# Kernel tuning notes

Hardware: AMD Instinct MI355X
Metric: run time of the kernel (lower is better)

## Reference

```python
import jax, jax.numpy as jnp
import numpy as np

D = 512       # d_model
M = 64        # working memory_dim
SE = 32       # episodic slots
SS = 64       # semantic slots
H = 4         # episodic heads
B, L = 2, 1024
BOT = max(D // 4, 32)  # controller bottleneck = 128


def _layernorm(x, g, b, eps=1e-5):
    mu = jnp.mean(x, axis=-1, keepdims=True)
    var = jnp.var(x, axis=-1, keepdims=True)
    return (x - mu) * jax.lax.rsqrt(var + eps) * g + b


def setup_inputs() -> dict:
    key = jax.random.key(0)
    ks = jax.random.split(key, 24)
    r = lambda i, shape, s=0.02: jax.random.normal(ks[i], shape, dtype=jnp.float32) * s
    return {
        "x": jax.random.normal(ks[0], (B, L, D), dtype=jnp.float32),
        # WorkingMemory (weights stored as (in, out))
        "Wq": r(1, (D, M)), "Wk": r(2, (D, M)), "Wv": r(3, (D, D)),
        "Wf": r(4, (D, M)), "bf": jnp.zeros((M,), jnp.float32),
        "Wo": r(5, (D, D)),
        "ln_g": jnp.ones((D,), jnp.float32), "ln_b": jnp.zeros((D,), jnp.float32),
        # EpisodicMemory
        "eslots": r(6, (1, SE, D)),
        "Eq": r(7, (D, D)), "Ek": r(8, (D, D)), "Ev": r(9, (D, D)), "Eo": r(10, (D, D)),
        # SemanticMemory
        "know": r(11, (1, SS, D)),
        "Sin": r(12, (D, D)),
        "Sg_w": r(13, (D, D)), "Sg_b": jnp.zeros((D,), jnp.float32),
        "So": r(14, (D, D)),
        # MemoryController
        "C1w": r(15, (D, BOT)), "C1b": jnp.zeros((BOT,), jnp.float32),
        "C2w": r(16, (BOT, 3)), "C2b": jnp.zeros((3,), jnp.float32),
    }


def _forward(x, Wq, Wk, Wv, Wf, bf, Wo, ln_g, ln_b,
             eslots, Eq, Ek, Ev, Eo,
             know, Sin, Sg_w, Sg_b, So,
             C1w, C1b, C2w, C2b):
    b, l, d = x.shape
    # ---- WorkingMemory (parallel gated linear attention) ----
    scale = M ** -0.5
    q = (jax.nn.elu(x @ Wq) + 1.0) * scale          # (B,L,M)
    k = jax.nn.elu(x @ Wk) + 1.0                    # (B,L,M)
    v = x @ Wv                                      # (B,L,D)
    forget = jax.nn.sigmoid(x @ Wf + bf)            # (B,L,M)
    log_f_cum = jnp.clip(jnp.cumsum(jnp.log(jnp.clip(forget, 1e-6, None)), axis=1), -20.0, 20.0)
    exp_neg = jnp.exp(-log_f_cum)
    exp_pos = jnp.exp(log_f_cum)
    kv = k[..., :, None] * v[..., None, :]          # (B,L,M,D) outer product
    cum_kv = jnp.cumsum(exp_neg[..., None] * kv, axis=1)
    Mstate = exp_pos[..., None] * cum_kv            # (B,L,M,D)
    z = exp_pos * jnp.cumsum(exp_neg * k, axis=1)   # (B,L,M)
    num = jnp.einsum('blm,blmd->bld', q, Mstate)
    den = jnp.einsum('blm,blm->bl', q, z)[..., None] + 1e-6
    w_out = _layernorm(num / den, ln_g, ln_b) @ Wo  # (B,L,D)

    # ---- EpisodicMemory (cross-attn to learned slots) ----
    hd = D // H
    mem = jnp.broadcast_to(eslots, (b, SE, D))
    qh = (x @ Eq).reshape(b, l, H, hd)
    kh = (mem @ Ek).reshape(b, SE, H, hd)
    vh = (mem @ Ev).reshape(b, SE, H, hd)
    scores = jnp.einsum('blhe,bshe->bhls', qh, kh) / jnp.sqrt(jnp.float32(hd))
    attn = jax.nn.softmax(scores, axis=-1)
    e_out = jnp.einsum('bhls,bshe->blhe', attn, vh).reshape(b, l, D) @ Eo

    # ---- SemanticMemory (single-head attn to knowledge, gated residual) ----
    kb = jnp.broadcast_to(know, (b, SS, D))
    qs = x @ Sin                                    # (B,L,D)
    s_scores = jnp.einsum('bld,bsd->bls', qs, kb) / jnp.sqrt(jnp.float32(D))
    s_attn = jax.nn.softmax(s_scores, axis=-1)
    retrieved = jnp.einsum('bls,bsd->bld', s_attn, kb)
    gate = jax.nn.sigmoid(x @ Sg_w + Sg_b)
    s_out = (gate * retrieved + (1.0 - gate) * x) @ So

    # ---- Controller fusion ----
    wts = jax.nn.softmax(jax.nn.silu(x @ C1w + C1b) @ C2w + C2b, axis=-1)  # (B,L,3)
    fused = (wts[..., 0:1] * w_out + wts[..., 1:2] * e_out + wts[..., 2:3] * s_out)
    return fused


def reference(x, Wq, Wk, Wv, Wf, bf, Wo, ln_g, ln_b,
              eslots, Eq, Ek, Ev, Eo,
              know, Sin, Sg_w, Sg_b, So,
              C1w, C1b, C2w, C2b):
    return _forward(x, Wq, Wk, Wv, Wf, bf, Wo, ln_g, ln_b,
                    eslots, Eq, Ek, Ev, Eo,
                    know, Sin, Sg_w, Sg_b, So,
                    C1w, C1b, C2w, C2b)
```

## Files before the change

### kernel.cpp

```cpp
#include <hip/hip_runtime.h>
#include <cstdint>

typedef unsigned int uint;
typedef unsigned short ushort;
typedef __attribute__((ext_vector_type(8))) short bf16x8;
typedef __attribute__((ext_vector_type(4))) float f32x4;

__device__ __forceinline__ ushort f2b(float f) {
  union { float f; uint u; } v; v.f = f;
  uint u = v.u;
  uint r = (u + 0x7FFFu + ((u >> 16) & 1u)) >> 16;
  return (ushort)r;
}
__device__ __forceinline__ float b2f(ushort h) {
  union { uint u; float f; } v; v.u = ((uint)h) << 16; return v.f;
}

__global__ __launch_bounds__(256) void k_prep(
    const float* __restrict__ x, const float* __restrict__ Wv, const float* __restrict__ Sg,
    const float* __restrict__ C1w, const float* __restrict__ Wq, const float* __restrict__ Wk,
    const float* __restrict__ Wo, const float* __restrict__ So, const float* __restrict__ know,
    const float* __restrict__ eslots, const float* __restrict__ Ek, const float* __restrict__ Ev,
    const float* __restrict__ Sin, const float* __restrict__ Wf, const float* __restrict__ bfb,
    ushort* __restrict__ X16, ushort* __restrict__ Wcat, ushort* __restrict__ Wfin,
    ushort* __restrict__ know16, float* __restrict__ kh, float* __restrict__ vh,
    float* __restrict__ logfb)
{
  __shared__ __align__(16) float Af[16 * 32];
  __shared__ __align__(16) float Bf[32 * 64];
  __shared__ __align__(16) float T[64][65];
  int bid = blockIdx.x;
  int tid = threadIdx.x;
  int lane = tid & 63, wv = tid >> 6;

  if (bid < 128) {
    int r0 = bid * 16;
    int row = tid >> 4, col4 = (tid & 15) * 4;
    float a0 = 0.f, a1 = 0.f, a2 = 0.f, a3 = 0.f;
    for (int kt = 0; kt < 16; ++kt) {
      if (tid < 128) {
        int p = tid; int rr = p >> 3, c4 = (p & 7) * 4;
        *(float4*)&Af[rr * 32 + c4] = *(const float4*)&x[(size_t)(r0 + rr) * 512 + kt * 32 + c4];
      }
      #pragma unroll
      for (int i = 0; i < 2; ++i) {
        int p = i * 256 + tid; int rr = p >> 4, c4 = (p & 15) * 4;
        *(float4*)&Bf[rr * 64 + c4] = *(const float4*)&Wf[(size_t)(kt * 32 + rr) * 64 + c4];
      }
      __syncthreads();
      #pragma unroll 8
      for (int ks = 0; ks < 32; ++ks) {
        float a = Af[row * 32 + ks];
        float4 b = *(float4*)&Bf[ks * 64 + col4];
        a0 += a * b.x; a1 += a * b.y; a2 += a * b.z; a3 += a * b.w;
      }
      __syncthreads();
    }
    float accs[4] = {a0, a1, a2, a3};
    #pragma unroll
    for (int j = 0; j < 4; ++j) {
      float logit = accs[j] + bfb[col4 + j];
      float s = 1.f / (1.f + expf(-logit));
      logfb[(size_t)(r0 + row) * 64 + col4 + j] = logf(fmaxf(s, 1e-6f));
    }
    return;
  }
  if (bid < 256) {
    int t = (bid - 128) * 256 + tid;
    if (t < 16384) {
      int s = t >> 9, j = t & 511;
      float acc = 0.f;
      #pragma unroll 8
      for (int d = 0; d < 512; ++d) acc += eslots[s * 512 + d] * Ek[d * 512 + j];
      kh[s * 512 + j] = acc;
    } else {
      int o = t - 16384; int s = o >> 9, j = o & 511;
      float acc = 0.f;
      #pragma unroll 8
      for (int d = 0; d < 512; ++d) acc += eslots[s * 512 + d] * Ev[d * 512 + j];
      vh[s * 512 + j] = acc;
    }
    return;
  }
  if (bid < 384) {
    int k = (bid - 256) * 4 + wv;
    const float* sp = Sin + (size_t)k * 512 + lane * 8;
    float4 s1 = *(const float4*)&sp[0];
    float4 s2 = *(const float4*)&sp[4];
    for (int s = 0; s < 64; ++s) {
      const float* kp = know + (size_t)s * 512 + lane * 8;
      float4 k1 = *(const float4*)&kp[0];
      float4 k2 = *(const float4*)&kp[4];
      float part = s1.x * k1.x + s1.y * k1.y + s1.z * k1.z + s1.w * k1.w
                 + s2.x * k2.x + s2.y * k2.y + s2.z * k2.z + s2.w * k2.w;
      #pragma unroll
      for (int o = 32; o; o >>= 1) part += __shfl_xor(part, o);
      if (lane == 0) Wcat[(640 + s) * 512 + k] = f2b(part * 0.04419417382415922f);
    }
    return;
  }
  if (bid < 672) {
    int tt = bid - 384;
    const float* src; ushort* dst; int sld, dld, Nt, drow, dcol;
    if (tt < 64)       {           src = Wv;  dst = Wcat; sld = 512; dld = 512;  Nt = 8; drow = 0;    dcol = 0;   }
    else if (tt < 128) { tt -= 64; src = Sg;  dst = Wcat; sld = 512; dld = 512;  Nt = 8; drow = 704;  dcol = 0;   }
    else if (tt < 144) { tt -= 128; src = C1w; dst = Wcat; sld = 128; dld = 512; Nt = 2; drow = 1216; dcol = 0;   }
    else if (tt < 152) { tt -= 144; src = Wq;  dst = Wcat; sld = 64;  dld = 512; Nt = 1; drow = 1344; dcol = 0;   }
    else if (tt < 160) { tt -= 152; src = Wk;  dst = Wcat; sld = 64;  dld = 512; Nt = 1; drow = 1408; dcol = 0;   }
    else if (tt < 224) { tt -= 160; src = Wo;  dst = Wfin; sld = 512; dld = 1152; Nt = 8; drow = 0;   dcol = 0;   }
    else               { tt -= 224; src = So;  dst = Wfin; sld = 512; dld = 1152; Nt = 8; drow = 0;   dcol = 512; }
    int tk = tt / Nt, tn = tt % Nt;
    int k0 = tk * 64, n0 = tn * 64;
    int r = tid >> 4, c = (tid & 15) * 4;
    #pragma unroll
    for (int p = 0; p < 4; ++p) {
      int kk = p * 16 + r;
      float4 v = *(const float4*)&src[(size_t)(k0 + kk) * sld + n0 + c];
      T[c + 0][kk] = v.x; T[c + 1][kk] = v.y; T[c + 2][kk] = v.z; T[c + 3][kk] = v.w;
    }
    __syncthreads();
    int n = tid >> 2, kc = (tid & 3) * 16;
    uint u[8];
    #pragma unroll
    for (int j = 0; j < 8; ++j) {
      ushort lo = f2b(T[n][kc + 2 * j]);
      ushort hi = f2b(T[n][kc + 2 * j + 1]);
      u[j] = (uint)lo | ((uint)hi << 16);
    }
    size_t off = (size_t)(drow + n0 + n) * dld + dcol + k0 + kc;
    uint4 o1; o1.x = u[0]; o1.y = u[1]; o1.z = u[2]; o1.w = u[3];
    uint4 o2; o2.x = u[4]; o2.y = u[5]; o2.z = u[6]; o2.w = u[7];
    *(uint4*)&dst[off] = o1;
    *(uint4*)&dst[off + 8] = o2;
    return;
  }
  if (bid < 800) {
    int base = (bid - 672) * 256 + tid;
    #pragma unroll
    for (int it = 0; it < 8; ++it) {
      int t = base + it * 32768;
      float4 xv = *(const float4*)&x[(size_t)t * 4];
      uint2 o;
      o.x = (uint)f2b(xv.x) | ((uint)f2b(xv.y) << 16);
      o.y = (uint)f2b(xv.z) | ((uint)f2b(xv.w) << 16);
      *(uint2*)&X16[(size_t)t * 4] = o;
    }
    return;
  }
  {
    int t = (bid - 800) * 256 + tid;
    #pragma unroll
    for (int j = 0; j < 2; ++j) {
      float4 v = *(const float4*)&know[(size_t)t * 8 + j * 4];
      uint2 o;
      o.x = (uint)f2b(v.x) | ((uint)f2b(v.y) << 16);
      o.y = (uint)f2b(v.z) | ((uint)f2b(v.w) << 16);
      *(uint2*)&know16[(size_t)t * 8 + j * 4] = o;
    }
  }
}

__global__ __launch_bounds__(256) void k_pre2(
    const float* __restrict__ Eq, const float* __restrict__ kh, const float* __restrict__ vh,
    const float* __restrict__ Eo, ushort* __restrict__ Wcat, ushort* __restrict__ Wfin)
{
  int bid = blockIdx.x;
  int tid = threadIdx.x;
  int lane = tid & 63, wv = tid >> 6;
  if (bid < 256) {
    int gw = bid * 4 + wv;
    #pragma unroll
    for (int pp = 0; pp < 2; ++pp) {
      int pair = gw * 2 + pp;
      int k = pair >> 2, h = pair & 3;
      const float* ep = Eq + (size_t)k * 512 + h * 128 + lane * 2;
      float e0 = ep[0], e1 = ep[1];
      for (int s = 0; s < 32; ++s) {
        const float* kp = kh + (size_t)s * 512 + h * 128 + lane * 2;
        float part = e0 * kp[0] + e1 * kp[1];
        #pragma unroll
        for (int o = 32; o; o >>= 1) part += __shfl_xor(part, o);
        if (lane == 0) Wcat[(512 + h * 32 + s) * 512 + k] = f2b(part * 0.08838834764831845f);
      }
    }
  } else {
    int o = (bid - 256) * 256 + tid;
    int hs = o >> 9, j = o & 511;
    int h = hs >> 5, s = hs & 31;
    const float* vhp = vh + (size_t)s * 512 + h * 128;
    float acc = 0.f;
    #pragma unroll 8
    for (int e = 0; e < 128; ++e) acc += vhp[e] * Eo[(size_t)(h * 128 + e) * 512 + j];
    Wfin[(size_t)j * 1152 + 1024 + hs] = f2b(acc);
  }
}

__global__ __launch_bounds__(256) void k_gemm1(
    const ushort* __restrict__ A, const ushort* __restrict__ Bw, float* __restrict__ C,
    const float* __restrict__ sgb, const float* __restrict__ c1b)
{
  __shared__ __align__(16) ushort As[64 * 32];
  __shared__ __align__(16) ushort Bs[128 * 32];
  int tid = threadIdx.x;
  int lane = tid & 63, wv = tid >> 6;
  int wm = (wv & 1) * 32, wn = (wv >> 1) * 64;
  int lr = lane & 15, lk = lane >> 4;
  int m0 = blockIdx.y * 64, n0 = blockIdx.x * 128;
  f32x4 zero4 = {0.f, 0.f, 0.f, 0.f};
  f32x4 acc[2][4];
  #pragma unroll
  for (int a = 0; a < 2; ++a)
    #pragma unroll
    for (int b = 0; b < 4; ++b) acc[a][b] = zero4;
  for (int kt = 0; kt < 16; ++kt) {
    int k0 = kt * 32;
    {
      int p = tid, row = p >> 2, cc = p & 3;
      int cs = cc ^ ((row >> 1) & 3);
      *(uint4*)&As[p * 8] = *(const uint4*)&A[(size_t)(m0 + row) * 512 + k0 + cs * 8];
    }
    #pragma unroll
    for (int i = 0; i < 2; ++i) {
      int p = i * 256 + tid, row = p >> 2, cc = p & 3;
      int cs = cc ^ ((row >> 1) & 3);
      *(uint4*)&Bs[p * 8] = *(const uint4*)&Bw[(size_t)(n0 + row) * 512 + k0 + cs * 8];
    }
    __syncthreads();
    bf16x8 af[2], bfv[4];
    #pragma unroll
    for (int mi = 0; mi < 2; ++mi) {
      int row = wm + mi * 16 + lr;
      int cc = lk ^ ((row >> 1) & 3);
      af[mi] = *(bf16x8*)&As[row * 32 + cc * 8];
    }
    #pragma unroll
    for (int ni = 0; ni < 4; ++ni) {
      int row = wn + ni * 16 + lr;
      int cc = lk ^ ((row >> 1) & 3);
      bfv[ni] = *(bf16x8*)&Bs[row * 32 + cc * 8];
    }
    #pragma unroll
    for (int mi = 0; mi < 2; ++mi)
      #pragma unroll
      for (int ni = 0; ni < 4; ++ni)
        acc[mi][ni] = __builtin_amdgcn_mfma_f32_16x16x32_bf16(af[mi], bfv[ni], acc[mi][ni], 0, 0, 0);
    __syncthreads();
  }
  #pragma unroll
  for (int mi = 0; mi < 2; ++mi) {
    #pragma unroll
    for (int ni = 0; ni < 4; ++ni) {
      int col = n0 + wn + ni * 16 + lr;
      #pragma unroll
      for (int r = 0; r < 4; ++r) {
        int rowb = m0 + wm + mi * 16 + lk * 4 + r;
        float v = acc[mi][ni][r];
        if (col >= 704) {
          if (col < 1216) { v = 1.f / (1.f + __expf(-(v + sgb[col - 704]))); }
          else if (col < 1344) { float tt = v + c1b[col - 1216]; v = tt / (1.f + __expf(-tt)); }
          else if (col < 1408) { float e = (v > 0.f) ? v : (__expf(v) - 1.f); v = (e + 1.f) * 0.125f; }
          else if (col < 1472) { float e = (v > 0.f) ? v : (__expf(v) - 1.f); v = e + 1.f; }
        }
        C[(size_t)rowb * 1536 + col] = v;
      }
    }
  }
}

__global__ __launch_bounds__(256) void k_gemm2(
    const ushort* __restrict__ A, const ushort* __restrict__ Bw, float* __restrict__ C)
{
  __shared__ __align__(16) ushort As[64 * 32];
  __shared__ __align__(16) ushort Bs[64 * 32];
  int tid = threadIdx.x;
  int lane = tid & 63, wv = tid >> 6;
  int wm = (wv & 1) * 32, wn = (wv >> 1) * 32;
  int lr = lane & 15, lk = lane >> 4;
  int m0 = blockIdx.y * 64, n0 = blockIdx.x * 64;
  f32x4 zero4 = {0.f, 0.f, 0.f, 0.f};
  f32x4 acc[2][2];
  #pragma unroll
  for (int a = 0; a < 2; ++a)
    #pragma unroll
    for (int b = 0; b < 2; ++b) acc[a][b] = zero4;
  for (int kt = 0; kt < 36; ++kt) {
    int k0 = kt * 32;
    {
      int p = tid, row = p >> 2, cc = p & 3;
      int cs = cc ^ ((row >> 1) & 3);
      *(uint4*)&As[p * 8] = *(const uint4*)&A[(size_t)(m0 + row) * 1152 + k0 + cs * 8];
      *(uint4*)&Bs[p * 8] = *(const uint4*)&Bw[(size_t)(n0 + row) * 1152 + k0 + cs * 8];
    }
    __syncthreads();
    bf16x8 af[2], bfv[2];
    #pragma unroll
    for (int mi = 0; mi < 2; ++mi) {
      int row = wm + mi * 16 + lr;
      int cc = lk ^ ((row >> 1) & 3);
      af[mi] = *(bf16x8*)&As[row * 32 + cc * 8];
    }
    #pragma unroll
    for (int ni = 0; ni < 2; ++ni) {
      int row = wn + ni * 16 + lr;
      int cc = lk ^ ((row >> 1) & 3);
      bfv[ni] = *(bf16x8*)&Bs[row * 32 + cc * 8];
    }
    #pragma unroll
    for (int mi = 0; mi < 2; ++mi)
      #pragma unroll
      for (int ni = 0; ni < 2; ++ni)
        acc[mi][ni] = __builtin_amdgcn_mfma_f32_16x16x32_bf16(af[mi], bfv[ni], acc[mi][ni], 0, 0, 0);
    __syncthreads();
  }
  #pragma unroll
  for (int mi = 0; mi < 2; ++mi) {
    #pragma unroll
    for (int ni = 0; ni < 2; ++ni) {
      int col = n0 + wn + ni * 16 + lr;
      #pragma unroll
      for (int r = 0; r < 4; ++r) {
        int rowb = m0 + wm + mi * 16 + lk * 4 + r;
        C[(size_t)rowb * 512 + col] = acc[mi][ni][r];
      }
    }
  }
}

__global__ __launch_bounds__(256) void k_gatescan(
    const float* __restrict__ logfb, const float* __restrict__ P,
    float* __restrict__ cn, float* __restrict__ qe, float* __restrict__ qz)
{
  __shared__ float wsumA[4];
  __shared__ float wsumB[4];
  int bidx = blockIdx.x;
  int b = bidx >> 6, m = bidx & 63;
  int tid = threadIdx.x;
  int lane = tid & 63, wv = tid >> 6;
  size_t rbase = (size_t)b * 1024 + tid * 4;

  float v0 = logfb[(rbase + 0) * 64 + m];
  float v1 = logfb[(rbase + 1) * 64 + m];
  float v2 = logfb[(rbase + 2) * 64 + m];
  float v3 = logfb[(rbase + 3) * 64 + m];
  v1 += v0; v2 += v1; v3 += v2;
  float tsum = v3;
  float sc = tsum;
  #pragma unroll
  for (int o = 1; o < 64; o <<= 1) {
    float t = __shfl_up(sc, o, 64);
    if (lane >= o) sc += t;
  }
  if (lane == 63) wsumA[wv] = sc;
  __syncthreads();
  float excl = sc - tsum;
  #pragma unroll
  for (int w2 = 0; w2 < 3; ++w2) if (w2 < wv) excl += wsumA[w2];

  float vv[4] = {v0, v1, v2, v3};
  float cv[4], qv[4];
  #pragma unroll
  for (int i = 0; i < 4; ++i) {
    size_t r = rbase + i;
    float lf = fminf(fmaxf(excl + vv[i], -20.f), 20.f);
    float en = expf(-lf), ep = expf(lf);
    float kk = P[r * 1536 + 1408 + m];
    float qq = P[r * 1536 + 1344 + m];
    cv[i] = en * kk;
    qv[i] = qq * ep;
    cn[r * 64 + m] = cv[i];
    qe[r * 64 + m] = qv[i];
  }

  float c1 = cv[0], c2 = c1 + cv[1], c3 = c2 + cv[2], c4 = c3 + cv[3];
  float t2 = c4;
  float sc2 = t2;
  #pragma unroll
  for (int o = 1; o < 64; o <<= 1) {
    float t = __shfl_up(sc2, o, 64);
    if (lane >= o) sc2 += t;
  }
  if (lane == 63) wsumB[wv] = sc2;
  __syncthreads();
  float excl2 = sc2 - t2;
  #pragma unroll
  for (int w2 = 0; w2 < 3; ++w2) if (w2 < wv) excl2 += wsumB[w2];

  float pr[4] = {c1, c2, c3, c4};
  #pragma unroll
  for (int i = 0; i < 4; ++i) {
    size_t r = rbase + i;
    qz[r * 64 + m] = qv[i] * (excl2 + pr[i]);
  }
}

__global__ __launch_bounds__(256) void k_scanA(
    const float* __restrict__ cn, const float* __restrict__ P, float* __restrict__ Send)
{
  __shared__ __align__(16) float cnS[16 * 64];
  __shared__ __align__(16) float vS[16 * 64];
  int tid = threadIdx.x;
  int bid = blockIdx.x;
  int dt = bid & 7, c = (bid >> 3) & 15, b = bid >> 7;
  int rb0 = b * 1024 + c * 64;
  int mg = tid >> 4, dl = tid & 15;
  float4 acc[4];
  #pragma unroll
  for (int i = 0; i < 4; ++i) acc[i] = make_float4(0.f, 0.f, 0.f, 0.f);
  for (int ig = 0; ig < 4; ++ig) {
    int rb = rb0 + ig * 16;
    int row = tid >> 4, c4f = (tid & 15) * 4;
    *(float4*)&cnS[row * 64 + c4f] = *(const float4*)&cn[(size_t)(rb + row) * 64 + c4f];
    *(float4*)&vS[row * 64 + c4f] = *(const float4*)&P[(size_t)(rb + row) * 1536 + dt * 64 + c4f];
    __syncthreads();
    #pragma unroll 4
    for (int i = 0; i < 16; ++i) {
      float4 vv = *(float4*)&vS[i * 64 + dl * 4];
      float4 cm = *(float4*)&cnS[i * 64 + mg * 4];
      acc[0].x += cm.x * vv.x; acc[0].y += cm.x * vv.y; acc[0].z += cm.x * vv.z; acc[0].w += cm.x * vv.w;
      acc[1].x += cm.y * vv.x; acc[1].y += cm.y * vv.y; acc[1].z += cm.y * vv.z; acc[1].w += cm.y * vv.w;
      acc[2].x += cm.z * vv.x; acc[2].y += cm.z * vv.y; acc[2].z += cm.z * vv.z; acc[2].w += cm.z * vv.w;
      acc[3].x += cm.w * vv.x; acc[3].y += cm.w * vv.y; acc[3].z += cm.w * vv.z; acc[3].w += cm.w * vv.w;
    }
    __syncthreads();
  }
  #pragma unroll
  for (int mi = 0; mi < 4; ++mi) {
    int m = mg * 4 + mi;
    *(float4*)&Send[(size_t)((b * 16 + c) * 64 + m) * 512 + dt * 64 + dl * 4] = acc[mi];
  }
}

__global__ __launch_bounds__(256) void k_scanB(const float* __restrict__ Send, float* __restrict__ carry)
{
  int t = blockIdx.x * 256 + threadIdx.x;
  int d = t & 511, m = (t >> 9) & 63, b = t >> 15;
  float run = 0.f;
  for (int c = 0; c < 16; ++c) {
    size_t idx = (size_t)((b * 16 + c) * 64 + m) * 512 + d;
    carry[idx] = run;
    run += Send[idx];
  }
}

__global__ __launch_bounds__(256) void k_scanC(
    const float* __restrict__ cn, const float* __restrict__ qe, const float* __restrict__ P,
    const float* __restrict__ carry, float* __restrict__ num)
{
  __shared__ __align__(16) float cnS[16 * 64];
  __shared__ __align__(16) float qeS[16 * 64];
  __shared__ __align__(16) float vS[16 * 64];
  int tid = threadIdx.x;
  int bid = blockIdx.x;
  int dt = bid & 7, c = (bid >> 3) & 15, b = bid >> 7;
  int rb0 = b * 1024 + c * 64;
  int mg = tid & 3, dl = tid >> 2;
  int d = dt * 64 + dl;
  float S[16];
  #pragma unroll
  for (int mi = 0; mi < 16; ++mi)
    S[mi] = carry[(size_t)((b * 16 + c) * 64 + mg * 16 + mi) * 512 + d];
  for (int ig = 0; ig < 4; ++ig) {
    int rb = rb0 + ig * 16;
    int row = tid >> 4, c4f = (tid & 15) * 4;
    *(float4*)&cnS[row * 64 + c4f] = *(const float4*)&cn[(size_t)(rb + row) * 64 + c4f];
    *(float4*)&qeS[row * 64 + c4f] = *(const float4*)&qe[(size_t)(rb + row) * 64 + c4f];
    *(float4*)&vS[row * 64 + c4f] = *(const float4*)&P[(size_t)(rb + row) * 1536 + dt * 64 + c4f];
    __syncthreads();
    for (int i = 0; i < 16; ++i) {
      float vv = vS[i * 64 + dl];
      float p = 0.f;
      #pragma unroll
      for (int j = 0; j < 4; ++j) {
        float4 c4 = *(float4*)&cnS[i * 64 + mg * 16 + j * 4];
        float4 q4 = *(float4*)&qeS[i * 64 + mg * 16 + j * 4];
        S[j * 4 + 0] += c4.x * vv; p += q4.x * S[j * 4 + 0];
        S[j * 4 + 1] += c4.y * vv; p += q4.y * S[j * 4 + 1];
        S[j * 4 + 2] += c4.z * vv; p += q4.z * S[j * 4 + 2];
        S[j * 4 + 3] += c4.w * vv; p += q4.w * S[j * 4 + 3];
      }
      p += __shfl_xor(p, 1);
      p += __shfl_xor(p, 2);
      if (mg == 0) num[(size_t)(rb + i) * 512 + d] = p;
    }
    __syncthreads();
  }
}

__global__ __launch_bounds__(256) void k_post(
    const float* __restrict__ P, const float* __restrict__ x,
    const float* __restrict__ num, const float* __restrict__ qz,
    const ushort* __restrict__ know16, const float* __restrict__ lng,
    const float* __restrict__ lnb, const float* __restrict__ C2w,
    const float* __restrict__ C2b, ushort* __restrict__ Afin)
{
  __shared__ __align__(16) ushort kbuf[32 * 512];
  __shared__ float attnL[4][64];
  __shared__ float w2L[4];
  int tid = threadIdx.x;
  int w = tid >> 6, lane = tid & 63;
  int r0 = blockIdx.x * 4;
  int r = r0 + w;
  size_t pr = (size_t)r * 1536;

  float h0 = P[pr + 1216 + lane], h1 = P[pr + 1280 + lane];
  float a0 = h0 * C2w[lane * 3 + 0] + h1 * C2w[(64 + lane) * 3 + 0];
  float a1 = h0 * C2w[lane * 3 + 1] + h1 * C2w[(64 + lane) * 3 + 1];
  float a2 = h0 * C2w[lane * 3 + 2] + h1 * C2w[(64 + lane) * 3 + 2];
  #pragma unroll
  for (int o = 32; o; o >>= 1) {
    a0 += __shfl_xor(a0, o); a1 += __shfl_xor(a1, o); a2 += __shfl_xor(a2, o);
  }
  a0 += C2b[0]; a1 += C2b[1]; a2 += C2b[2];
  float mxc = fmaxf(a0, fmaxf(a1, a2));
  float e0 = expf(a0 - mxc), e1 = expf(a1 - mxc), e2c = expf(a2 - mxc);
  float inv = 1.f / (e0 + e1 + e2c);
  float w0 = e0 * inv, w1 = e1 * inv, w2 = e2c * inv;
  if (lane == 0) w2L[w] = w2;

  {
    float den = qz[(size_t)r * 64 + lane];
    #pragma unroll
    for (int o = 32; o; o >>= 1) den += __shfl_xor(den, o);
    den += 1e-6f;
    float y[8];
    float4 n0 = *(const float4*)&num[(size_t)r * 512 + lane * 8];
    float4 n1 = *(const float4*)&num[(size_t)r * 512 + lane * 8 + 4];
    y[0] = n0.x / den; y[1] = n0.y / den; y[2] = n0.z / den; y[3] = n0.w / den;
    y[4] = n1.x / den; y[5] = n1.y / den; y[6] = n1.z / den; y[7] = n1.w / den;
    float s1 = 0.f, s2 = 0.f;
    #pragma unroll
    for (int i = 0; i < 8; ++i) { s1 += y[i]; s2 += y[i] * y[i]; }
    #pragma unroll
    for (int o = 32; o; o >>= 1) { s1 += __shfl_xor(s1, o); s2 += __shfl_xor(s2, o); }
    float mu = s1 * (1.f / 512.f);
    float var = s2 * (1.f / 512.f) - mu * mu;
    float rs = rsqrtf(var + 1e-5f);
    uint4 outv;
    uint pk[4];
    #pragma unroll
    for (int p2 = 0; p2 < 4; ++p2) {
      float o0 = (y[2 * p2] - mu) * rs * lng[lane * 8 + 2 * p2] + lnb[lane * 8 + 2 * p2];
      float o1 = (y[2 * p2 + 1] - mu) * rs * lng[lane * 8 + 2 * p2 + 1] + lnb[lane * 8 + 2 * p2 + 1];
      pk[p2] = (uint)f2b(o0 * w0) | ((uint)f2b(o1 * w0) << 16);
    }
    outv.x = pk[0]; outv.y = pk[1]; outv.z = pk[2]; outv.w = pk[3];
    *(uint4*)&Afin[(size_t)r * 1152 + lane * 8] = outv;
  }

  {
    int h = lane >> 4, ei = (lane & 15) * 2;
    float v0 = P[pr + 512 + h * 32 + ei], v1 = P[pr + 512 + h * 32 + ei + 1];
    float mxe = fmaxf(v0, v1);
    #pragma unroll
    for (int o = 1; o < 16; o <<= 1) mxe = fmaxf(mxe, __shfl_xor(mxe, o));
    float ee0 = __expf(v0 - mxe), ee1 = __expf(v1 - mxe);
    float ss = ee0 + ee1;
    #pragma unroll
    for (int o = 1; o < 16; o <<= 1) ss += __shfl_xor(ss, o);
    float sc1 = w1 / ss;
    uint pkv = (uint)f2b(ee0 * sc1) | ((uint)f2b(ee1 * sc1) << 16);
    *(uint*)&Afin[(size_t)r * 1152 + 1024 + h * 32 + ei] = pkv;
  }

  {
    float lv = P[pr + 640 + lane];
    float mx = lv;
    #pragma unroll
    for (int o = 32; o; o >>= 1) mx = fmaxf(mx, __shfl_xor(mx, o));
    float e = __expf(lv - mx);
    float sum = e;
    #pragma unroll
    for (int o = 32; o; o >>= 1) sum += __shfl_xor(sum, o);
    attnL[w][lane] = e / sum;
  }

  int dd = tid * 2;
  float acc[4][2];
  #pragma unroll
  for (int i = 0; i < 4; ++i) { acc[i][0] = 0.f; acc[i][1] = 0.f; }
  for (int hs = 0; hs < 2; ++hs) {
    #pragma unroll
    for (int i = 0; i < 8; ++i) {
      int idx = i * 256 + tid;
      *(uint4*)&kbuf[idx * 8] = *(const uint4*)&know16[(size_t)hs * 16384 + idx * 8];
    }
    __syncthreads();
    for (int s = 0; s < 32; ++s) {
      uint uu = *(uint*)&kbuf[s * 512 + dd];
      float k0 = b2f((ushort)(uu & 0xffff));
      float k1 = b2f((ushort)(uu >> 16));
      #pragma unroll
      for (int row = 0; row < 4; ++row) {
        float a = attnL[row][hs * 32 + s];
        acc[row][0] += a * k0;
        acc[row][1] += a * k1;
      }
    }
    __syncthreads();
  }
  #pragma unroll
  for (int row = 0; row < 4; ++row) {
    int rr = r0 + row;
    float g0 = P[(size_t)rr * 1536 + 704 + dd];
    float g1 = P[(size_t)rr * 1536 + 704 + dd + 1];
    float x0 = x[(size_t)rr * 512 + dd], x1 = x[(size_t)rr * 512 + dd + 1];
    float w2v = w2L[row];
    float m0 = g0 * acc[row][0] + (1.f - g0) * x0;
    float m1 = g1 * acc[row][1] + (1.f - g1) * x1;
    uint pkv = (uint)f2b(w2v * m0) | ((uint)f2b(w2v * m1) << 16);
    *(uint*)&Afin[(size_t)rr * 1152 + 512 + dd] = pkv;
  }
}

extern "C" void kernel_launch(void* const* d_in, const int* in_sizes, int n_in,
                              void* d_out, int out_size, void* d_ws, size_t ws_size,
                              hipStream_t stream)
{
  const float* x     = (const float*)d_in[0];
  const float* Wq    = (const float*)d_in[1];
  const float* Wk    = (const float*)d_in[2];
  const float* Wv    = (const float*)d_in[3];
  const float* Wf    = (const float*)d_in[4];
  const float* bfb   = (const float*)d_in[5];
  const float* Wo    = (const float*)d_in[6];
  const float* ln_g  = (const float*)d_in[7];
  const float* ln_b  = (const float*)d_in[8];
  const float* eslots= (const float*)d_in[9];
  const float* Eq    = (const float*)d_in[10];
  const float* Ek    = (const float*)d_in[11];
  const float* Ev    = (const float*)d_in[12];
  const float* Eo    = (const float*)d_in[13];
  const float* know  = (const float*)d_in[14];
  const float* Sin   = (const float*)d_in[15];
  const float* Sg_w  = (const float*)d_in[16];
  const float* Sg_b  = (const float*)d_in[17];
  const float* So    = (const float*)d_in[18];
  const float* C1w   = (const float*)d_in[19];
  const float* C1b   = (const float*)d_in[20];
  const float* C2w   = (const float*)d_in[21];
  const float* C2b   = (const float*)d_in[22];

  char* ws = (char*)d_ws;
  ushort* X16    = (ushort*)(ws + 0);
  ushort* Wcat   = (ushort*)(ws + 2097152);
  ushort* Wfin   = (ushort*)(ws + 3670016);
  ushort* know16 = (ushort*)(ws + 4849664);
  float*  kh     = (float*)(ws + 4915200);
  float*  vh     = (float*)(ws + 4980736);
  float*  P      = (float*)(ws + 5046272);
  float*  logfb  = (float*)(ws + 17629184);
  float*  cn     = (float*)(ws + 18153472);
  float*  qe     = (float*)(ws + 18677760);
  float*  qz     = (float*)(ws + 19202048);
  float*  Send   = (float*)(ws + 19726336);
  float*  carry  = (float*)(ws + 23920640);
  float*  num    = (float*)(ws + 28114944);
  ushort* Afin   = (ushort*)(ws + 32342016);

  k_prep<<<dim3(816), dim3(256), 0, stream>>>(x, Wv, Sg_w, C1w, Wq, Wk, Wo, So, know,
                                              eslots, Ek, Ev, Sin, Wf, bfb,
                                              X16, Wcat, Wfin, know16, kh, vh, logfb);
  k_pre2<<<dim3(512), dim3(256), 0, stream>>>(Eq, kh, vh, Eo, Wcat, Wfin);
  k_gemm1<<<dim3(12, 32), dim3(256), 0, stream>>>(X16, Wcat, P, Sg_b, C1b);
  k_gatescan<<<dim3(128), dim3(256), 0, stream>>>(logfb, P, cn, qe, qz);
  k_scanA<<<dim3(256), dim3(256), 0, stream>>>(cn, P, Send);
  k_scanB<<<dim3(256), dim3(256), 0, stream>>>(Send, carry);
  k_scanC<<<dim3(256), dim3(256), 0, stream>>>(cn, qe, P, carry, num);
  k_post<<<dim3(512), dim3(256), 0, stream>>>(P, x, num, qz, know16, ln_g, ln_b, C2w, C2b, Afin);
  k_gemm2<<<dim3(8, 32), dim3(256), 0, stream>>>(Afin, Wfin, (float*)d_out);
}
```

Measured before the change: 145.3 us.

## Fuse gate scan into chunked scan kernels and drop carry pass

```diff
diff --git a/kernel.cpp b/kernel.cpp
--- a/kernel.cpp
+++ b/kernel.cpp
@@ -24,7 +24,7 @@
     const float* __restrict__ Sin, const float* __restrict__ Wf, const float* __restrict__ bfb,
     ushort* __restrict__ X16, ushort* __restrict__ Wcat, ushort* __restrict__ Wfin,
     ushort* __restrict__ know16, float* __restrict__ kh, float* __restrict__ vh,
-    float* __restrict__ logfb)
+    float* __restrict__ logfb, float* __restrict__ s16)
 {
   __shared__ __align__(16) float Af[16 * 32];
   __shared__ __align__(16) float Bf[32 * 64];
@@ -57,11 +57,22 @@
       __syncthreads();
     }
     float accs[4] = {a0, a1, a2, a3};
+    float lv[4];
     #pragma unroll
     for (int j = 0; j < 4; ++j) {
       float logit = accs[j] + bfb[col4 + j];
       float s = 1.f / (1.f + expf(-logit));
-      logfb[(size_t)(r0 + row) * 64 + col4 + j] = logf(fmaxf(s, 1e-6f));
+      lv[j] = logf(fmaxf(s, 1e-6f));
+      logfb[(size_t)(r0 + row) * 64 + col4 + j] = lv[j];
+    }
+    #pragma unroll
+    for (int j = 0; j < 4; ++j) Bf[row * 64 + col4 + j] = lv[j];
+    __syncthreads();
+    if (tid < 64) {
+      float s = 0.f;
+      #pragma unroll
+      for (int rr = 0; rr < 16; ++rr) s += Bf[rr * 64 + tid];
+      s16[(size_t)bid * 64 + tid] = s;
     }
     return;
   }
@@ -326,82 +337,38 @@
   }
 }
 
-__global__ __launch_bounds__(256) void k_gatescan(
-    const float* __restrict__ logfb, const float* __restrict__ P,
-    float* __restrict__ cn, float* __restrict__ qe, float* __restrict__ qz)
-{
-  __shared__ float wsumA[4];
-  __shared__ float wsumB[4];
-  int bidx = blockIdx.x;
-  int b = bidx >> 6, m = bidx & 63;
-  int tid = threadIdx.x;
-  int lane = tid & 63, wv = tid >> 6;
-  size_t rbase = (size_t)b * 1024 + tid * 4;
-
-  float v0 = logfb[(rbase + 0) * 64 + m];
-  float v1 = logfb[(rbase + 1) * 64 + m];
-  float v2 = logfb[(rbase + 2) * 64 + m];
-  float v3 = logfb[(rbase + 3) * 64 + m];
-  v1 += v0; v2 += v1; v3 += v2;
-  float tsum = v3;
-  float sc = tsum;
-  #pragma unroll
-  for (int o = 1; o < 64; o <<= 1) {
-    float t = __shfl_up(sc, o, 64);
-    if (lane >= o) sc += t;
-  }
-  if (lane == 63) wsumA[wv] = sc;
-  __syncthreads();
-  float excl = sc - tsum;
-  #pragma unroll
-  for (int w2 = 0; w2 < 3; ++w2) if (w2 < wv) excl += wsumA[w2];
-
-  float vv[4] = {v0, v1, v2, v3};
-  float cv[4], qv[4];
-  #pragma unroll
-  for (int i = 0; i < 4; ++i) {
-    size_t r = rbase + i;
-    float lf = fminf(fmaxf(excl + vv[i], -20.f), 20.f);
-    float en = expf(-lf), ep = expf(lf);
-    float kk = P[r * 1536 + 1408 + m];
-    float qq = P[r * 1536 + 1344 + m];
-    cv[i] = en * kk;
-    qv[i] = qq * ep;
-    cn[r * 64 + m] = cv[i];
-    qe[r * 64 + m] = qv[i];
-  }
-
-  float c1 = cv[0], c2 = c1 + cv[1], c3 = c2 + cv[2], c4 = c3 + cv[3];
-  float t2 = c4;
-  float sc2 = t2;
-  #pragma unroll
-  for (int o = 1; o < 64; o <<= 1) {
-    float t = __shfl_up(sc2, o, 64);
-    if (lane >= o) sc2 += t;
-  }
-  if (lane == 63) wsumB[wv] = sc2;
-  __syncthreads();
-  float excl2 = sc2 - t2;
-  #pragma unroll
-  for (int w2 = 0; w2 < 3; ++w2) if (w2 < wv) excl2 += wsumB[w2];
-
-  float pr[4] = {c1, c2, c3, c4};
-  #pragma unroll
-  for (int i = 0; i < 4; ++i) {
-    size_t r = rbase + i;
-    qz[r * 64 + m] = qv[i] * (excl2 + pr[i]);
-  }
-}
-
 __global__ __launch_bounds__(256) void k_scanA(
-    const float* __restrict__ cn, const float* __restrict__ P, float* __restrict__ Send)
-{
-  __shared__ __align__(16) float cnS[16 * 64];
+    const float* __restrict__ logfb, const float* __restrict__ s16,
+    const float* __restrict__ P, float* __restrict__ Send, float* __restrict__ zSend)
+{
+  __shared__ __align__(16) float cnS[64 * 64];
+  __shared__ __align__(16) float kS[64 * 64];
   __shared__ __align__(16) float vS[16 * 64];
   int tid = threadIdx.x;
   int bid = blockIdx.x;
   int dt = bid & 7, c = (bid >> 3) & 15, b = bid >> 7;
   int rb0 = b * 1024 + c * 64;
+  for (int idx = tid; idx < 1024; idx += 256) {
+    int i = idx >> 4, m4 = (idx & 15) * 4;
+    *(float4*)&cnS[i * 64 + m4] = *(const float4*)&logfb[(size_t)(rb0 + i) * 64 + m4];
+    *(float4*)&kS[i * 64 + m4] = *(const float4*)&P[(size_t)(rb0 + i) * 1536 + 1408 + m4];
+  }
+  __syncthreads();
+  if (tid < 64) {
+    int m = tid;
+    float run = 0.f;
+    for (int j = 0; j < c * 4; ++j) run += s16[(size_t)(b * 64 + j) * 64 + m];
+    float zs = 0.f;
+    for (int i = 0; i < 64; ++i) {
+      run += cnS[i * 64 + m];
+      float lf = fminf(fmaxf(run, -20.f), 20.f);
+      float cv = __expf(-lf) * kS[i * 64 + m];
+      cnS[i * 64 + m] = cv;
+      zs += cv;
+    }
+    if (dt == 0) zSend[(size_t)(b * 16 + c) * 64 + m] = zs;
+  }
+  __syncthreads();
   int mg = tid >> 4, dl = tid & 15;
   float4 acc[4];
   #pragma unroll
@@ -409,13 +376,12 @@
   for (int ig = 0; ig < 4; ++ig) {
     int rb = rb0 + ig * 16;
     int row = tid >> 4, c4f = (tid & 15) * 4;
-    *(float4*)&cnS[row * 64 + c4f] = *(const float4*)&cn[(size_t)(rb + row) * 64 + c4f];
     *(float4*)&vS[row * 64 + c4f] = *(const float4*)&P[(size_t)(rb + row) * 1536 + dt * 64 + c4f];
     __syncthreads();
     #pragma unroll 4
     for (int i = 0; i < 16; ++i) {
       float4 vv = *(float4*)&vS[i * 64 + dl * 4];
-      float4 cm = *(float4*)&cnS[i * 64 + mg * 4];
+      float4 cm = *(float4*)&cnS[(ig * 16 + i) * 64 + mg * 4];
       acc[0].x += cm.x * vv.x; acc[0].y += cm.x * vv.y; acc[0].z += cm.x * vv.z; acc[0].w += cm.x * vv.w;
       acc[1].x += cm.y * vv.x; acc[1].y += cm.y * vv.y; acc[1].z += cm.y * vv.z; acc[1].w += cm.y * vv.w;
       acc[2].x += cm.z * vv.x; acc[2].y += cm.z * vv.y; acc[2].z += cm.z * vv.z; acc[2].w += cm.z * vv.w;
@@ -430,57 +396,86 @@
   }
 }
 
-__global__ __launch_bounds__(256) void k_scanB(const float* __restrict__ Send, float* __restrict__ carry)
-{
-  int t = blockIdx.x * 256 + threadIdx.x;
-  int d = t & 511, m = (t >> 9) & 63, b = t >> 15;
-  float run = 0.f;
-  for (int c = 0; c < 16; ++c) {
-    size_t idx = (size_t)((b * 16 + c) * 64 + m) * 512 + d;
-    carry[idx] = run;
-    run += Send[idx];
-  }
-}
-
 __global__ __launch_bounds__(256) void k_scanC(
-    const float* __restrict__ cn, const float* __restrict__ qe, const float* __restrict__ P,
-    const float* __restrict__ carry, float* __restrict__ num)
-{
-  __shared__ __align__(16) float cnS[16 * 64];
-  __shared__ __align__(16) float qeS[16 * 64];
+    const float* __restrict__ logfb, const float* __restrict__ s16,
+    const float* __restrict__ P, const float* __restrict__ Send,
+    const float* __restrict__ zSend, float* __restrict__ num, float* __restrict__ den)
+{
+  __shared__ __align__(16) float cnS[64 * 64];
+  __shared__ __align__(16) float qeS[64 * 64];
+  __shared__ __align__(16) float kS[64 * 64];
   __shared__ __align__(16) float vS[16 * 64];
   int tid = threadIdx.x;
   int bid = blockIdx.x;
   int dt = bid & 7, c = (bid >> 3) & 15, b = bid >> 7;
   int rb0 = b * 1024 + c * 64;
+  for (int idx = tid; idx < 1024; idx += 256) {
+    int i = idx >> 4, m4 = (idx & 15) * 4;
+    *(float4*)&cnS[i * 64 + m4] = *(const float4*)&logfb[(size_t)(rb0 + i) * 64 + m4];
+    *(float4*)&kS[i * 64 + m4] = *(const float4*)&P[(size_t)(rb0 + i) * 1536 + 1408 + m4];
+    *(float4*)&qeS[i * 64 + m4] = *(const float4*)&P[(size_t)(rb0 + i) * 1536 + 1344 + m4];
+  }
+  __syncthreads();
+  if (tid < 64) {
+    int m = tid;
+    float run = 0.f;
+    for (int j = 0; j < c * 4; ++j) run += s16[(size_t)(b * 64 + j) * 64 + m];
+    for (int i = 0; i < 64; ++i) {
+      run += cnS[i * 64 + m];
+      float lf = fminf(fmaxf(run, -20.f), 20.f);
+      float ep = __expf(lf), en = __expf(-lf);
+      cnS[i * 64 + m] = en * kS[i * 64 + m];
+      qeS[i * 64 + m] = qeS[i * 64 + m] * ep;
+    }
+  }
+  __syncthreads();
   int mg = tid & 3, dl = tid >> 2;
   int d = dt * 64 + dl;
   float S[16];
-  #pragma unroll
-  for (int mi = 0; mi < 16; ++mi)
-    S[mi] = carry[(size_t)((b * 16 + c) * 64 + mg * 16 + mi) * 512 + d];
+  float z16[16];
+  #pragma unroll
+  for (int mi = 0; mi < 16; ++mi) { S[mi] = 0.f; z16[mi] = 0.f; }
+  for (int j = 0; j < c; ++j) {
+    size_t base = (size_t)((b * 16 + j) * 64 + mg * 16) * 512 + d;
+    #pragma unroll
+    for (int mi = 0; mi < 16; ++mi) S[mi] += Send[base + (size_t)mi * 512];
+    size_t zb = (size_t)(b * 16 + j) * 64 + mg * 16;
+    #pragma unroll
+    for (int mi = 0; mi < 16; ++mi) z16[mi] += zSend[zb + mi];
+  }
   for (int ig = 0; ig < 4; ++ig) {
     int rb = rb0 + ig * 16;
     int row = tid >> 4, c4f = (tid & 15) * 4;
-    *(float4*)&cnS[row * 64 + c4f] = *(const float4*)&cn[(size_t)(rb + row) * 64 + c4f];
-    *(float4*)&qeS[row * 64 + c4f] = *(const float4*)&qe[(size_t)(rb + row) * 64 + c4f];
     *(float4*)&vS[row * 64 + c4f] = *(const float4*)&P[(size_t)(rb + row) * 1536 + dt * 64 + c4f];
     __syncthreads();
     for (int i = 0; i < 16; ++i) {
+      int ii = ig * 16 + i;
       float vv = vS[i * 64 + dl];
       float p = 0.f;
+      float dp = 0.f;
       #pragma unroll
       for (int j = 0; j < 4; ++j) {
-        float4 c4 = *(float4*)&cnS[i * 64 + mg * 16 + j * 4];
-        float4 q4 = *(float4*)&qeS[i * 64 + mg * 16 + j * 4];
+        float4 c4 = *(float4*)&cnS[ii * 64 + mg * 16 + j * 4];
+        float4 q4 = *(float4*)&qeS[ii * 64 + mg * 16 + j * 4];
         S[j * 4 + 0] += c4.x * vv; p += q4.x * S[j * 4 + 0];
         S[j * 4 + 1] += c4.y * vv; p += q4.y * S[j * 4 + 1];
         S[j * 4 + 2] += c4.z * vv; p += q4.z * S[j * 4 + 2];
         S[j * 4 + 3] += c4.w * vv; p += q4.w * S[j * 4 + 3];
+        if (dt == 0) {
+          z16[j * 4 + 0] += c4.x; dp += q4.x * z16[j * 4 + 0];
+          z16[j * 4 + 1] += c4.y; dp += q4.y * z16[j * 4 + 1];
+          z16[j * 4 + 2] += c4.z; dp += q4.z * z16[j * 4 + 2];
+          z16[j * 4 + 3] += c4.w; dp += q4.w * z16[j * 4 + 3];
+        }
       }
       p += __shfl_xor(p, 1);
       p += __shfl_xor(p, 2);
-      if (mg == 0) num[(size_t)(rb + i) * 512 + d] = p;
+      if (mg == 0) num[(size_t)(rb0 + ii) * 512 + d] = p;
+      if (dt == 0) {
+        dp += __shfl_xor(dp, 1);
+        dp += __shfl_xor(dp, 2);
+        if (mg == 0 && dl == 0) den[rb0 + ii] = dp;
+      }
     }
     __syncthreads();
   }
@@ -488,7 +483,7 @@
 
 __global__ __launch_bounds__(256) void k_post(
     const float* __restrict__ P, const float* __restrict__ x,
-    const float* __restrict__ num, const float* __restrict__ qz,
+    const float* __restrict__ num, const float* __restrict__ denB,
     const ushort* __restrict__ know16, const float* __restrict__ lng,
     const float* __restrict__ lnb, const float* __restrict__ C2w,
     const float* __restrict__ C2b, ushort* __restrict__ Afin)
@@ -518,15 +513,12 @@
   if (lane == 0) w2L[w] = w2;
 
   {
-    float den = qz[(size_t)r * 64 + lane];
-    #pragma unroll
-    for (int o = 32; o; o >>= 1) den += __shfl_xor(den, o);
-    den += 1e-6f;
+    float dv = denB[r] + 1e-6f;
     float y[8];
     float4 n0 = *(const float4*)&num[(size_t)r * 512 + lane * 8];
     float4 n1 = *(const float4*)&num[(size_t)r * 512 + lane * 8 + 4];
-    y[0] = n0.x / den; y[1] = n0.y / den; y[2] = n0.z / den; y[3] = n0.w / den;
-    y[4] = n1.x / den; y[5] = n1.y / den; y[6] = n1.z / den; y[7] = n1.w / den;
+    y[0] = n0.x / dv; y[1] = n0.y / dv; y[2] = n0.z / dv; y[3] = n0.w / dv;
+    y[4] = n1.x / dv; y[5] = n1.y / dv; y[6] = n1.z / dv; y[7] = n1.w / dv;
     float s1 = 0.f, s2 = 0.f;
     #pragma unroll
     for (int i = 0; i < 8; ++i) { s1 += y[i]; s2 += y[i] * y[i]; }
@@ -649,23 +641,20 @@
   float*  vh     = (float*)(ws + 4980736);
   float*  P      = (float*)(ws + 5046272);
   float*  logfb  = (float*)(ws + 17629184);
-  float*  cn     = (float*)(ws + 18153472);
-  float*  qe     = (float*)(ws + 18677760);
-  float*  qz     = (float*)(ws + 19202048);
+  float*  s16    = (float*)(ws + 18153472);
+  float*  zSend  = (float*)(ws + 18677760);
+  float*  den    = (float*)(ws + 19202048);
   float*  Send   = (float*)(ws + 19726336);
-  float*  carry  = (float*)(ws + 23920640);
   float*  num    = (float*)(ws + 28114944);
   ushort* Afin   = (ushort*)(ws + 32342016);
 
   k_prep<<<dim3(816), dim3(256), 0, stream>>>(x, Wv, Sg_w, C1w, Wq, Wk, Wo, So, know,
                                               eslots, Ek, Ev, Sin, Wf, bfb,
-                                              X16, Wcat, Wfin, know16, kh, vh, logfb);
+                                              X16, Wcat, Wfin, know16, kh, vh, logfb, s16);
   k_pre2<<<dim3(512), dim3(256), 0, stream>>>(Eq, kh, vh, Eo, Wcat, Wfin);
   k_gemm1<<<dim3(12, 32), dim3(256), 0, stream>>>(X16, Wcat, P, Sg_b, C1b);
-  k_gatescan<<<dim3(128), dim3(256), 0, stream>>>(logfb, P, cn, qe, qz);
-  k_scanA<<<dim3(256), dim3(256), 0, stream>>>(cn, P, Send);
-  k_scanB<<<dim3(256), dim3(256), 0, stream>>>(Send, carry);
-  k_scanC<<<dim3(256), dim3(256), 0, stream>>>(cn, qe, P, carry, num);
-  k_post<<<dim3(512), dim3(256), 0, stream>>>(P, x, num, qz, know16, ln_g, ln_b, C2w, C2b, Afin);
+  k_scanA<<<dim3(256), dim3(256), 0, stream>>>(logfb, s16, P, Send, zSend);
+  k_scanC<<<dim3(256), dim3(256), 0, stream>>>(logfb, s16, P, Send, zSend, num, den);
+  k_post<<<dim3(512), dim3(256), 0, stream>>>(P, x, num, den, know16, ln_g, ln_b, C2w, C2b, Afin);
   k_gemm2<<<dim3(8, 32), dim3(256), 0, stream>>>(Afin, Wfin, (float*)d_out);
 }
```

New measurement: 182.9 us. 25.9% more time.
